# Kernel tuning notes

Measured on AMD Instinct MI355X. Metric: run time of the kernel, lower is better.

## Reference

```python
import jax, jax.numpy as jnp
import numpy as np

HEAD_NUM = 16
KEY_DIM = 64
EMBED = 1024
KV_OUT = HEAD_NUM * KEY_DIM  # 1024


def setup_inputs() -> dict:
    key = jax.random.key(0)
    ks = jax.random.split(key, 11)
    B, L, E = 2, 2048, EMBED
    scale = 0.02
    return {
        "query": jax.random.normal(ks[0], (B, L, E), jnp.float32),
        "key": jax.random.normal(ks[1], (B, L, E), jnp.float32),
        "value": jax.random.normal(ks[2], (B, L, E), jnp.float32),
        "W_Query": jax.random.normal(ks[3], (E, KV_OUT), jnp.float32) * scale,
        "W_Key": jax.random.normal(ks[4], (E, KV_OUT), jnp.float32) * scale,
        "W_Value": jax.random.normal(ks[5], (E, KV_OUT), jnp.float32) * scale,
        "W_Output": jax.random.normal(ks[6], (KV_OUT, E), jnp.float32) * scale,
        "B_Query": jnp.zeros((KV_OUT,), jnp.float32),
        "B_Key": jnp.zeros((KV_OUT,), jnp.float32),
        "B_Value": jnp.zeros((KV_OUT,), jnp.float32),
        "B_Output": jnp.zeros((E,), jnp.float32),
    }


def reference(query, key, value, W_Query, W_Key, W_Value, W_Output,
              B_Query, B_Key, B_Value, B_Output):
    B, Lq, E = query.shape
    Lk = key.shape[1]
    H, D = HEAD_NUM, KEY_DIM
    # QKV projections + bias
    q = query @ W_Query + B_Query            # [B, Lq, H*D]
    k = key @ W_Key + B_Key                  # [B, Lk, H*D]
    v = value @ W_Value + B_Value            # [B, Lk, H*D]
    # tf.split(axis=2) per head == reshape to [B, L, H, D]
    q = q.reshape(B, Lq, H, D)
    k = k.reshape(B, Lk, H, D)
    v = v.reshape(B, Lk, H, D)
    # scaled dot-product attention (no mask, dropout=0)
    scores = jnp.einsum("bqhd,bkhd->bhqk", q, k) / (D ** 0.5)
    probs = jax.nn.softmax(scores, axis=-1)
    out = jnp.einsum("bhqk,bkhd->bqhd", probs, v)  # [B, Lq, H, D]
    out = out.reshape(B, Lq, H * D)
    return out @ W_Output + B_Output
```

## Files before the change

kernel.cpp:

```cpp
#include <hip/hip_runtime.h>

using u16 = unsigned short;
using u32 = unsigned int;

typedef __attribute__((ext_vector_type(8))) short bf16x8;
typedef __attribute__((ext_vector_type(4))) float f32x4;
typedef __attribute__((ext_vector_type(4))) u32 u32x4;
typedef __attribute__((ext_vector_type(2))) u32 u32x2;
typedef __attribute__((ext_vector_type(4))) _Float16 f16x4;

#define MFMA_BF16_K32(a, b, c) __builtin_amdgcn_mfma_f32_16x16x32_bf16((a), (b), (c), 0, 0, 0)
#define MFMA_F16_K16(a, b, c) __builtin_amdgcn_mfma_f32_16x16x16f16((a), (b), (c), 0, 0, 0)

#define QSCALE 0.18033688011112042f

extern "C" __device__ float __ocml_native_exp2_f32(float);

__device__ __forceinline__ u16 f2bf(float f) {
  u32 u = __builtin_bit_cast(u32, f);
  return (u16)((u + 0x7fffu + ((u >> 16) & 1u)) >> 16);
}

__device__ __forceinline__ u32 pk_f16(float a, float b) {
  auto v = __builtin_amdgcn_cvt_pkrtz(a, b);
  return __builtin_bit_cast(u32, v);
}

__device__ __forceinline__ void load_lds16(const void* g, void* l) {
  __builtin_amdgcn_global_load_lds((__attribute__((address_space(1))) void*)g,
                                   (__attribute__((address_space(3))) void*)l,
                                   16, 0, 0);
}

__global__ __launch_bounds__(256) void cvt_all_kernel(
    const float* __restrict__ q, const float* __restrict__ k, const float* __restrict__ v,
    u16* __restrict__ oq, u16* __restrict__ ok, u16* __restrict__ ov,
    const float* __restrict__ w0, const float* __restrict__ w1,
    const float* __restrict__ w2, const float* __restrict__ w3,
    u16* __restrict__ d0, u16* __restrict__ d1,
    u16* __restrict__ d2, u16* __restrict__ d3) {
  const int id = blockIdx.x;
  const int tid = threadIdx.x;
  if (id < 6144) {
    const int z = id >> 11, bx = id & 2047;
    const float* s = z == 0 ? q : z == 1 ? k : v;
    u16* d = z == 0 ? oq : z == 1 ? ok : ov;
    int i = (bx * 256 + tid) * 8;
    f32x4 a = *(const f32x4*)(s + i);
    f32x4 b = *(const f32x4*)(s + i + 4);
    u32x4 o;
    o.x = (u32)f2bf(a.x) | ((u32)f2bf(a.y) << 16);
    o.y = (u32)f2bf(a.z) | ((u32)f2bf(a.w) << 16);
    o.z = (u32)f2bf(b.x) | ((u32)f2bf(b.y) << 16);
    o.w = (u32)f2bf(b.z) | ((u32)f2bf(b.w) << 16);
    *(u32x4*)(d + i) = o;
    return;
  }
  __shared__ float t[64][65];
  const int r0 = id - 6144;
  const int z = r0 >> 8, rr0 = r0 & 255;
  const int bx = rr0 & 15, by = rr0 >> 4;
  const float* src = z == 0 ? w0 : z == 1 ? w1 : z == 2 ? w2 : w3;
  u16* dst = z == 0 ? d0 : z == 1 ? d1 : z == 2 ? d2 : d3;
  const float scale = (z == 0) ? QSCALE : 1.0f;
  const int r = tid >> 4, c4 = (tid & 15) * 4;
#pragma unroll
  for (int i = 0; i < 4; ++i) {
    int row = r + i * 16;
    f32x4 vv = *(const f32x4*)(src + (by * 64 + row) * 1024 + bx * 64 + c4);
    t[row][c4 + 0] = vv.x;
    t[row][c4 + 1] = vv.y;
    t[row][c4 + 2] = vv.z;
    t[row][c4 + 3] = vv.w;
  }
  __syncthreads();
  const int rw = tid >> 2, cc = (tid & 3) * 16;
  alignas(16) u16 tmp[16];
#pragma unroll
  for (int j = 0; j < 16; ++j) tmp[j] = f2bf(t[cc + j][rw] * scale);
  u32x4* outp = (u32x4*)(dst + (bx * 64 + rw) * 1024 + by * 64 + cc);
  outp[0] = *(const u32x4*)&tmp[0];
  outp[1] = *(const u32x4*)&tmp[8];
}

__global__ __launch_bounds__(256) void gemm_qkv_kernel(
    const u16* __restrict__ x0, const u16* __restrict__ x1, const u16* __restrict__ x2,
    const u16* __restrict__ w0, const u16* __restrict__ w1, const u16* __restrict__ w2,
    const float* __restrict__ b0, const float* __restrict__ b1, const float* __restrict__ b2,
    u16* __restrict__ c0, u16* __restrict__ c1, u16* __restrict__ vt) {
  __shared__ u16 As[128 * 64];
  __shared__ u16 Bs[128 * 64];
  const int lid = blockIdx.x;
  const int xcd = lid & 7, rr = lid >> 3;
  const int nb = rr & 7, slot = rr >> 3;
  const int g = slot * 8 + xcd;
  const int z = g >> 5, m_idx = g & 31;
  const u16* A = z == 0 ? x0 : z == 1 ? x1 : x2;
  const u16* Bt = z == 0 ? w0 : z == 1 ? w1 : w2;
  const float* bias = z == 0 ? b0 : z == 1 ? b1 : b2;
  const float bscale = z == 0 ? QSCALE : 1.0f;
  const int tid = threadIdx.x;
  const int wave = tid >> 6, lane = tid & 63;
  const int l16 = lane & 15, quad = lane >> 4;
  const int l7 = l16 & 7;
  const int wm = wave >> 1, wn = wave & 1;
  const int m0 = m_idx * 128, n0 = nb * 128;

  f32x4 acc[4][4];
  const f32x4 zf = {0.f, 0.f, 0.f, 0.f};
#pragma unroll
  for (int i = 0; i < 4; ++i)
#pragma unroll
    for (int j = 0; j < 4; ++j) acc[i][j] = zf;

  for (int kb = 0; kb < 1024; kb += 64) {
#pragma unroll
    for (int t = 0; t < 4; ++t) {
      int c = wave * 256 + t * 64 + lane;
      int row = c >> 3, sc8 = (c & 7) ^ (row & 7);
      load_lds16(A + (m0 + row) * 1024 + kb + sc8 * 8, &As[(wave * 256 + t * 64) * 8]);
    }
#pragma unroll
    for (int t = 0; t < 4; ++t) {
      int c = wave * 256 + t * 64 + lane;
      int row = c >> 3, sc8 = (c & 7) ^ (row & 7);
      load_lds16(Bt + (n0 + row) * 1024 + kb + sc8 * 8, &Bs[(wave * 256 + t * 64) * 8]);
    }
    asm volatile("s_waitcnt vmcnt(0)" ::: "memory");
    __syncthreads();
#pragma unroll
    for (int ks = 0; ks < 2; ++ks) {
      const int sch = (ks * 4 + quad) ^ l7;
      bf16x8 af[4], bfv[4];
#pragma unroll
      for (int mt = 0; mt < 4; ++mt)
        af[mt] = *(const bf16x8*)&As[(wm * 64 + mt * 16 + l16) * 64 + sch * 8];
#pragma unroll
      for (int nt = 0; nt < 4; ++nt)
        bfv[nt] = *(const bf16x8*)&Bs[(wn * 64 + nt * 16 + l16) * 64 + sch * 8];
#pragma unroll
      for (int mt = 0; mt < 4; ++mt)
#pragma unroll
        for (int nt = 0; nt < 4; ++nt) acc[mt][nt] = MFMA_BF16_K32(af[mt], bfv[nt], acc[mt][nt]);
    }
    __syncthreads();
  }

  float bv[4];
#pragma unroll
  for (int nt = 0; nt < 4; ++nt) bv[nt] = bias[n0 + wn * 64 + nt * 16 + l16] * bscale;
  if (z != 2) {
    u16* C = z == 0 ? c0 : c1;
#pragma unroll
    for (int mt = 0; mt < 4; ++mt)
#pragma unroll
      for (int nt = 0; nt < 4; ++nt)
#pragma unroll
        for (int r = 0; r < 4; ++r) {
          int row = m0 + wm * 64 + mt * 16 + quad * 4 + r;
          int col = n0 + wn * 64 + nt * 16 + l16;
          C[row * 1024 + col] = f2bf(acc[mt][nt][r] + bv[nt]);
        }
  } else {
#pragma unroll
    for (int mt = 0; mt < 4; ++mt)
#pragma unroll
      for (int nt = 0; nt < 4; ++nt)
#pragma unroll
        for (int r = 0; r < 4; ++r) {
          int row = m0 + wm * 64 + mt * 16 + quad * 4 + r;
          int col = n0 + wn * 64 + nt * 16 + l16;
          int bb = row >> 11, kv = row & 2047;
          _Float16 hv = (_Float16)(acc[mt][nt][r] + bv[nt]);
          vt[(bb * 1024 + col) * 2048 + kv] = __builtin_bit_cast(u16, hv);
        }
  }
}

__global__ __launch_bounds__(256) void gemm_out_kernel(const u16* __restrict__ A,
                                                       const u16* __restrict__ Bt,
                                                       const float* __restrict__ bias,
                                                       float* __restrict__ C) {
  __shared__ u16 As[64 * 64];
  __shared__ u16 Bs[128 * 64];
  const int lid = blockIdx.x;
  const int xcd = lid & 7, rr = lid >> 3;
  const int nb = rr & 7, slot = rr >> 3;
  const int by = slot * 8 + xcd;
  const int tid = threadIdx.x;
  const int wave = tid >> 6, lane = tid & 63;
  const int l16 = lane & 15, quad = lane >> 4;
  const int l7 = l16 & 7;
  const int m0 = by * 64, n0 = nb * 128;

  f32x4 acc[4][2];
  const f32x4 zf = {0.f, 0.f, 0.f, 0.f};
#pragma unroll
  for (int i = 0; i < 4; ++i)
#pragma unroll
    for (int j = 0; j < 2; ++j) acc[i][j] = zf;

  for (int kb = 0; kb < 1024; kb += 64) {
#pragma unroll
    for (int t = 0; t < 2; ++t) {
      int c = wave * 128 + t * 64 + lane;
      int row = c >> 3, sc8 = (c & 7) ^ (row & 7);
      load_lds16(A + (m0 + row) * 1024 + kb + sc8 * 8, &As[(wave * 128 + t * 64) * 8]);
    }
#pragma unroll
    for (int t = 0; t < 4; ++t) {
      int c = wave * 256 + t * 64 + lane;
      int row = c >> 3, sc8 = (c & 7) ^ (row & 7);
      load_lds16(Bt + (n0 + row) * 1024 + kb + sc8 * 8, &Bs[(wave * 256 + t * 64) * 8]);
    }
    asm volatile("s_waitcnt vmcnt(0)" ::: "memory");
    __syncthreads();
#pragma unroll
    for (int ks = 0; ks < 2; ++ks) {
      const int sch = (ks * 4 + quad) ^ l7;
      bf16x8 af[4], bfv[2];
#pragma unroll
      for (int mt = 0; mt < 4; ++mt)
        af[mt] = *(const bf16x8*)&As[(mt * 16 + l16) * 64 + sch * 8];
#pragma unroll
      for (int nt = 0; nt < 2; ++nt)
        bfv[nt] = *(const bf16x8*)&Bs[(wave * 32 + nt * 16 + l16) * 64 + sch * 8];
#pragma unroll
      for (int mt = 0; mt < 4; ++mt)
#pragma unroll
        for (int nt = 0; nt < 2; ++nt) acc[mt][nt] = MFMA_BF16_K32(af[mt], bfv[nt], acc[mt][nt]);
    }
    __syncthreads();
  }

  float bv[2];
#pragma unroll
  for (int nt = 0; nt < 2; ++nt) bv[nt] = bias[n0 + wave * 32 + nt * 16 + l16];
#pragma unroll
  for (int mt = 0; mt < 4; ++mt)
#pragma unroll
    for (int nt = 0; nt < 2; ++nt)
#pragma unroll
      for (int r = 0; r < 4; ++r) {
        int row = m0 + mt * 16 + quad * 4 + r;
        int col = n0 + wave * 32 + nt * 16 + l16;
        C[row * 1024 + col] = acc[mt][nt][r] + bv[nt];
      }
}

__global__ __launch_bounds__(256, 2) void flash_kernel(const u16* __restrict__ Q,
                                                       const u16* __restrict__ K,
                                                       const u16* __restrict__ Vt,
                                                       u16* __restrict__ O) {
  __shared__ u16 k_lds[128 * 64];
  __shared__ u16 vt_lds[64 * 128];
  __shared__ float lred[4][64];
  __shared__ float lfin[64];
  const int tid = threadIdx.x;
  const int wave = tid >> 6, lane = tid & 63;
  const int l16 = lane & 15, quad = lane >> 4;
  const int l7 = l16 & 7;
  const int id = blockIdx.x;
  const int xcd = id & 7, slot = id >> 3;
  const int pair = xcd * 4 + (slot & 3);
  const int qb = slot >> 2;
  const int b = pair >> 4, h = pair & 15;
  const u16* Qh = Q + (b * 2048 + qb * 64) * 1024 + h * 64;
  const u16* Kh = K + b * 2048 * 1024 + h * 64;
  const u16* Vh = Vt + pair * 64 * 2048;

#pragma unroll
  for (int t = 0; t < 2; ++t) {
    int c = (t * 4 + wave) * 64 + lane;
    int row = c >> 3, sc8 = (c & 7) ^ (row & 7);
    load_lds16(Qh + row * 1024 + sc8 * 8, &k_lds[((t * 4 + wave) * 64) * 8]);
  }
  asm volatile("s_waitcnt vmcnt(0)" ::: "memory");
  __syncthreads();
  bf16x8 qf[4][2];
#pragma unroll
  for (int qn = 0; qn < 4; ++qn)
#pragma unroll
    for (int ks = 0; ks < 2; ++ks)
      qf[qn][ks] = *(const bf16x8*)&k_lds[(qn * 16 + l16) * 64 + (((ks * 4 + quad) ^ l7)) * 8];
  __syncthreads();

  f32x4 o_acc[4][4];
  const f32x4 zf = {0.f, 0.f, 0.f, 0.f};
#pragma unroll
  for (int qn = 0; qn < 4; ++qn)
#pragma unroll
    for (int dt = 0; dt < 4; ++dt) o_acc[qn][dt] = zf;
  float lp[4] = {0.f, 0.f, 0.f, 0.f};

  for (int kb = 0; kb < 16; ++kb) {
    const int kv0 = kb * 128;
#pragma unroll
    for (int t = 0; t < 4; ++t) {
      int c = (t * 4 + wave) * 64 + lane;
      int row = c >> 3, sc8 = (c & 7) ^ (row & 7);
      load_lds16(Kh + (kv0 + row) * 1024 + sc8 * 8, &k_lds[((t * 4 + wave) * 64) * 8]);
    }
#pragma unroll
    for (int t = 0; t < 4; ++t) {
      int c = (t * 4 + wave) * 64 + lane;
      int d = c >> 4, sc = (c & 15) ^ (d & 15);
      load_lds16(Vh + d * 2048 + kv0 + sc * 8, &vt_lds[((t * 4 + wave) * 64) * 8]);
    }
    asm volatile("s_waitcnt vmcnt(0)" ::: "memory");
    __syncthreads();

#pragma unroll
    for (int c2 = 0; c2 < 2; ++c2) {
      const int chunk = wave * 2 + c2;
      f32x4 s_acc[4];
#pragma unroll
      for (int qn = 0; qn < 4; ++qn) s_acc[qn] = zf;
#pragma unroll
      for (int ks = 0; ks < 2; ++ks) {
        bf16x8 kf = *(const bf16x8*)&k_lds[(chunk * 16 + l16) * 64 + ((ks * 4 + quad) ^ l7) * 8];
#pragma unroll
        for (int qn = 0; qn < 4; ++qn) s_acc[qn] = MFMA_BF16_K32(kf, qf[qn][ks], s_acc[qn]);
      }
      union { u32 u[2]; f16x4 v; } pkv[4];
#pragma unroll
      for (int qn = 0; qn < 4; ++qn) {
        float e0 = __ocml_native_exp2_f32(s_acc[qn].x);
        float e1 = __ocml_native_exp2_f32(s_acc[qn].y);
        float e2 = __ocml_native_exp2_f32(s_acc[qn].z);
        float e3 = __ocml_native_exp2_f32(s_acc[qn].w);
        lp[qn] += (e0 + e1) + (e2 + e3);
        pkv[qn].u[0] = pk_f16(e0, e1);
        pkv[qn].u[1] = pk_f16(e2, e3);
      }
#pragma unroll
      for (int dt = 0; dt < 4; ++dt) {
        f16x4 vf = *(const f16x4*)&vt_lds[(dt * 16 + l16) * 128 +
                                          (((chunk * 2 + (quad >> 1)) ^ l16) * 8) + (quad & 1) * 4];
#pragma unroll
        for (int qn = 0; qn < 4; ++qn)
          o_acc[qn][dt] = MFMA_F16_K16(pkv[qn].v, vf, o_acc[qn][dt]);
      }
    }
    __syncthreads();
  }

#pragma unroll
  for (int qn = 0; qn < 4; ++qn) {
    lp[qn] += __shfl_xor(lp[qn], 16);
    lp[qn] += __shfl_xor(lp[qn], 32);
  }
  if (quad == 0) {
#pragma unroll
    for (int qn = 0; qn < 4; ++qn) lred[wave][qn * 16 + l16] = lp[qn];
  }
  float* bufA = (float*)k_lds;
  float* bufB = (float*)vt_lds;
  if (wave == 1 || wave == 3) {
    float* buf = (wave == 1) ? bufA : bufB;
#pragma unroll
    for (int qm = 0; qm < 4; ++qm)
#pragma unroll
      for (int dt = 0; dt < 4; ++dt)
        *(f32x4*)&buf[(((qm * 4 + dt) * 4 + quad) * 16 + l16) * 4] = o_acc[qm][dt];
  }
  __syncthreads();
  if (tid < 64) lfin[tid] = lred[0][tid] + lred[1][tid] + lred[2][tid] + lred[3][tid];
  if (wave == 0 || wave == 2) {
    float* buf = (wave == 0) ? bufA : bufB;
#pragma unroll
    for (int qm = 0; qm < 4; ++qm)
#pragma unroll
      for (int dt = 0; dt < 4; ++dt)
        o_acc[qm][dt] += *(const f32x4*)&buf[(((qm * 4 + dt) * 4 + quad) * 16 + l16) * 4];
  }
  __syncthreads();
  if (wave == 2) {
#pragma unroll
    for (int qm = 0; qm < 4; ++qm)
#pragma unroll
      for (int dt = 0; dt < 4; ++dt)
        *(f32x4*)&bufA[(((qm * 4 + dt) * 4 + quad) * 16 + l16) * 4] = o_acc[qm][dt];
  }
  __syncthreads();
  if (wave == 0) {
#pragma unroll
    for (int qm = 0; qm < 4; ++qm)
#pragma unroll
      for (int dt = 0; dt < 4; ++dt)
        o_acc[qm][dt] += *(const f32x4*)&bufA[(((qm * 4 + dt) * 4 + quad) * 16 + l16) * 4];
#pragma unroll
    for (int qm = 0; qm < 4; ++qm)
#pragma unroll
      for (int r = 0; r < 4; ++r) {
        int qrow = qm * 16 + quad * 4 + r;
        float inv = 1.0f / lfin[qrow];
        int row = b * 2048 + qb * 64 + qrow;
#pragma unroll
        for (int dt = 0; dt < 4; ++dt)
          O[row * 1024 + h * 64 + dt * 16 + l16] = f2bf(o_acc[qm][dt][r] * inv);
      }
  }
}

extern "C" void kernel_launch(void* const* d_in, const int* in_sizes, int n_in,
                              void* d_out, int out_size, void* d_ws, size_t ws_size,
                              hipStream_t stream) {
  const float* q = (const float*)d_in[0];
  const float* k = (const float*)d_in[1];
  const float* v = (const float*)d_in[2];
  const float* Wq = (const float*)d_in[3];
  const float* Wk = (const float*)d_in[4];
  const float* Wv = (const float*)d_in[5];
  const float* Wo = (const float*)d_in[6];
  const float* Bq = (const float*)d_in[7];
  const float* Bk = (const float*)d_in[8];
  const float* Bv = (const float*)d_in[9];
  const float* Bo = (const float*)d_in[10];
  float* out = (float*)d_out;

  char* w = (char*)d_ws;
  const size_t MB = 1u << 20;
  u16* xq = (u16*)(w + 0 * MB);
  u16* xk = (u16*)(w + 8 * MB);
  u16* xv = (u16*)(w + 16 * MB);
  u16* wqt = (u16*)(w + 24 * MB);
  u16* wkt = (u16*)(w + 26 * MB);
  u16* wvt = (u16*)(w + 28 * MB);
  u16* wot = (u16*)(w + 30 * MB);
  u16* Qp = (u16*)(w + 32 * MB);
  u16* Kp = (u16*)(w + 40 * MB);
  u16* Vtr = (u16*)(w + 48 * MB);
  u16* At = (u16*)(w + 56 * MB);

  cvt_all_kernel<<<dim3(7168), 256, 0, stream>>>(q, k, v, xq, xk, xv,
                                                 Wq, Wk, Wv, Wo, wqt, wkt, wvt, wot);
  gemm_qkv_kernel<<<dim3(768), 256, 0, stream>>>(xq, xk, xv, wqt, wkt, wvt,
                                                 Bq, Bk, Bv, Qp, Kp, Vtr);
  flash_kernel<<<dim3(1024), 256, 0, stream>>>(Qp, Kp, Vtr, At);
  gemm_out_kernel<<<dim3(512), 256, 0, stream>>>(At, wot, Bo, out);
}
```

Baseline: 227.3 us.

## Double-buffer K/V tiles in flash kernel with async prefetch two blocks ahead

Splits the K and V^T shared-memory tiles into two buffers. The loads for block kb+2 are issued right after block kb's compute, and the loop waits with a partial vmcnt so global-to-LDS transfers overlap the MFMA work. It also raises wave priority around the MFMA groups with s_setprio. The cost is doubled LDS use, 64 KB for the tiles, which may limit the two-blocks-per-CU occupancy, and the vmcnt(8) count must match exactly the eight loads issued per block.

```diff
diff --git a/kernel.cpp b/kernel.cpp
--- a/kernel.cpp
+++ b/kernel.cpp
@@ -252,8 +252,8 @@
                                                        const u16* __restrict__ K,
                                                        const u16* __restrict__ Vt,
                                                        u16* __restrict__ O) {
-  __shared__ u16 k_lds[128 * 64];
-  __shared__ u16 vt_lds[64 * 128];
+  __shared__ u16 k_lds[2][128 * 64];
+  __shared__ u16 vt_lds[2][64 * 128];
   __shared__ float lred[4][64];
   __shared__ float lfin[64];
   const int tid = threadIdx.x;
@@ -273,7 +273,7 @@
   for (int t = 0; t < 2; ++t) {
     int c = (t * 4 + wave) * 64 + lane;
     int row = c >> 3, sc8 = (c & 7) ^ (row & 7);
-    load_lds16(Qh + row * 1024 + sc8 * 8, &k_lds[((t * 4 + wave) * 64) * 8]);
+    load_lds16(Qh + row * 1024 + sc8 * 8, &k_lds[0][((t * 4 + wave) * 64) * 8]);
   }
   asm volatile("s_waitcnt vmcnt(0)" ::: "memory");
   __syncthreads();
@@ -282,33 +282,42 @@
   for (int qn = 0; qn < 4; ++qn)
 #pragma unroll
     for (int ks = 0; ks < 2; ++ks)
-      qf[qn][ks] = *(const bf16x8*)&k_lds[(qn * 16 + l16) * 64 + (((ks * 4 + quad) ^ l7)) * 8];
-  __syncthreads();
-
-  f32x4 o_acc[4][4];
-  const f32x4 zf = {0.f, 0.f, 0.f, 0.f};
-#pragma unroll
-  for (int qn = 0; qn < 4; ++qn)
-#pragma unroll
-    for (int dt = 0; dt < 4; ++dt) o_acc[qn][dt] = zf;
-  float lp[4] = {0.f, 0.f, 0.f, 0.f};
-
-  for (int kb = 0; kb < 16; ++kb) {
-    const int kv0 = kb * 128;
+      qf[qn][ks] = *(const bf16x8*)&k_lds[0][(qn * 16 + l16) * 64 + (((ks * 4 + quad) ^ l7)) * 8];
+  __syncthreads();
+
+#pragma unroll
+  for (int bufi = 0; bufi < 2; ++bufi) {
+    const int kv0 = bufi * 128;
 #pragma unroll
     for (int t = 0; t < 4; ++t) {
       int c = (t * 4 + wave) * 64 + lane;
       int row = c >> 3, sc8 = (c & 7) ^ (row & 7);
-      load_lds16(Kh + (kv0 + row) * 1024 + sc8 * 8, &k_lds[((t * 4 + wave) * 64) * 8]);
+      load_lds16(Kh + (kv0 + row) * 1024 + sc8 * 8, &k_lds[bufi][((t * 4 + wave) * 64) * 8]);
     }
 #pragma unroll
     for (int t = 0; t < 4; ++t) {
       int c = (t * 4 + wave) * 64 + lane;
       int d = c >> 4, sc = (c & 15) ^ (d & 15);
-      load_lds16(Vh + d * 2048 + kv0 + sc * 8, &vt_lds[((t * 4 + wave) * 64) * 8]);
-    }
-    asm volatile("s_waitcnt vmcnt(0)" ::: "memory");
-    __syncthreads();
+      load_lds16(Vh + d * 2048 + kv0 + sc * 8, &vt_lds[bufi][((t * 4 + wave) * 64) * 8]);
+    }
+  }
+
+  f32x4 o_acc[4][4];
+  const f32x4 zf = {0.f, 0.f, 0.f, 0.f};
+#pragma unroll
+  for (int qn = 0; qn < 4; ++qn)
+#pragma unroll
+    for (int dt = 0; dt < 4; ++dt) o_acc[qn][dt] = zf;
+  float lp[4] = {0.f, 0.f, 0.f, 0.f};
+
+  for (int kb = 0; kb < 16; ++kb) {
+    const int cur = kb & 1;
+    if (kb < 15)
+      asm volatile("s_waitcnt vmcnt(8)" ::: "memory");
+    else
+      asm volatile("s_waitcnt vmcnt(0)" ::: "memory");
+    __builtin_amdgcn_s_barrier();
+    asm volatile("" ::: "memory");
 
 #pragma unroll
     for (int c2 = 0; c2 < 2; ++c2) {
@@ -318,9 +327,12 @@
       for (int qn = 0; qn < 4; ++qn) s_acc[qn] = zf;
 #pragma unroll
       for (int ks = 0; ks < 2; ++ks) {
-        bf16x8 kf = *(const bf16x8*)&k_lds[(chunk * 16 + l16) * 64 + ((ks * 4 + quad) ^ l7) * 8];
+        bf16x8 kf =
+            *(const bf16x8*)&k_lds[cur][(chunk * 16 + l16) * 64 + ((ks * 4 + quad) ^ l7) * 8];
+        __builtin_amdgcn_s_setprio(1);
 #pragma unroll
         for (int qn = 0; qn < 4; ++qn) s_acc[qn] = MFMA_BF16_K32(kf, qf[qn][ks], s_acc[qn]);
+        __builtin_amdgcn_s_setprio(0);
       }
       union { u32 u[2]; f16x4 v; } pkv[4];
 #pragma unroll
@@ -335,14 +347,34 @@
       }
 #pragma unroll
       for (int dt = 0; dt < 4; ++dt) {
-        f16x4 vf = *(const f16x4*)&vt_lds[(dt * 16 + l16) * 128 +
-                                          (((chunk * 2 + (quad >> 1)) ^ l16) * 8) + (quad & 1) * 4];
+        f16x4 vf = *(const f16x4*)&vt_lds[cur][(dt * 16 + l16) * 128 +
+                                               (((chunk * 2 + (quad >> 1)) ^ l16) * 8) +
+                                               (quad & 1) * 4];
+        __builtin_amdgcn_s_setprio(1);
 #pragma unroll
         for (int qn = 0; qn < 4; ++qn)
           o_acc[qn][dt] = MFMA_F16_K16(pkv[qn].v, vf, o_acc[qn][dt]);
-      }
-    }
-    __syncthreads();
+        __builtin_amdgcn_s_setprio(0);
+      }
+    }
+
+    __builtin_amdgcn_s_barrier();
+    asm volatile("" ::: "memory");
+    if (kb + 2 < 16) {
+      const int kv0 = (kb + 2) * 128;
+#pragma unroll
+      for (int t = 0; t < 4; ++t) {
+        int c = (t * 4 + wave) * 64 + lane;
+        int row = c >> 3, sc8 = (c & 7) ^ (row & 7);
+        load_lds16(Kh + (kv0 + row) * 1024 + sc8 * 8, &k_lds[cur][((t * 4 + wave) * 64) * 8]);
+      }
+#pragma unroll
+      for (int t = 0; t < 4; ++t) {
+        int c = (t * 4 + wave) * 64 + lane;
+        int d = c >> 4, sc = (c & 15) ^ (d & 15);
+        load_lds16(Vh + d * 2048 + kv0 + sc * 8, &vt_lds[cur][((t * 4 + wave) * 64) * 8]);
+      }
+    }
   }
 
 #pragma unroll
@@ -354,8 +386,8 @@
 #pragma unroll
     for (int qn = 0; qn < 4; ++qn) lred[wave][qn * 16 + l16] = lp[qn];
   }
-  float* bufA = (float*)k_lds;
-  float* bufB = (float*)vt_lds;
+  float* bufA = (float*)&k_lds[0][0];
+  float* bufB = (float*)&k_lds[1][0];
   if (wave == 1 || wave == 3) {
     float* buf = (wave == 1) ? bufA : bufB;
 #pragma unroll
```

Result: no change. 231.2 us (+1.7%).
